# Performance work log

Measured on AMD Instinct MI355X. Metric: run time of the kernel, lower is better.

Reference implementation:

```python
import jax, jax.numpy as jnp
import numpy as np

N, F_IN, H, OUT, E = 32000, 256, 4, 64, 512000
NEG_SLOPE = 0.2


def setup_inputs() -> dict:
    key = jax.random.key(0)
    ks = jax.random.split(key, 7)
    return {
        "feat": jax.random.normal(ks[0], (N, F_IN), dtype=jnp.float32),
        "dist": jax.random.uniform(ks[1], (E, 1, 1), dtype=jnp.float32),
        "W": jax.random.normal(ks[2], (F_IN, H * OUT), dtype=jnp.float32) * (1.0 / np.sqrt(F_IN)),
        "w_att_src": jax.random.normal(ks[3], (1, H, OUT), dtype=jnp.float32) * 0.1,
        "w_att_dst": jax.random.normal(ks[4], (1, H, OUT), dtype=jnp.float32) * 0.1,
        "src": jax.random.randint(ks[5], (E,), 0, N, dtype=jnp.int32),
        "dst": jax.random.randint(ks[6], (E,), 0, N, dtype=jnp.int32),
    }


def reference(feat, dist, W, w_att_src, w_att_dst, src, dst):
    n = feat.shape[0]
    # dense projection (no bias, no activation) then split heads: [N, H, OUT]
    ft = (feat @ W).reshape(n, H, OUT)
    # per-node attention logits: [N, H, 1]
    e_src = jnp.sum(ft * w_att_src, axis=-1, keepdims=True)
    e_dst = jnp.sum(ft * w_att_dst, axis=-1, keepdims=True)
    # edge logits via u_add_v gather: [E, H, 1]
    e = e_src[src] + e_dst[dst]
    e = jnp.where(e >= 0, e, NEG_SLOPE * e)  # leaky relu
    # edge softmax normalized over incoming edges of each dst node
    emax = jax.ops.segment_max(e, dst, num_segments=n)          # [N, H, 1]
    ex = jnp.exp(e - emax[dst])
    denom = jax.ops.segment_sum(ex, dst, num_segments=n)        # [N, H, 1]
    a = (ex / denom[dst]) * dist                                # [E, H, 1]
    # message = u_mul_e, aggregate = sum over incoming edges
    m = ft[src] * a                                             # [E, H, OUT]
    out = jax.ops.segment_sum(m, dst, num_segments=n)           # [N, H, OUT]
    return out.reshape(n, H * OUT)
```

## Files before the change

### kernel.cpp

```cpp
#include <hip/hip_runtime.h>

#define F_IN 256
#define NHEAD 4
#define DOUT 64
#define FOUT 256
#define NEG_SLOPE 0.2f
#define BCAP 64
#define PREP_BLKS 16
#define QSTRIDE 272

typedef __attribute__((ext_vector_type(8))) short bf16x8;
typedef __attribute__((ext_vector_type(4))) float f32x4;

__device__ __forceinline__ unsigned short f2bf(float x) {
    unsigned u = __float_as_uint(x);
    return (unsigned short)((u + 0x7FFFu + ((u >> 16) & 1u)) >> 16);
}

__global__ __launch_bounds__(256) void k_prep_zero(
    const float* __restrict__ W, unsigned short* __restrict__ Wt,
    int* __restrict__ cnt, int n)
{
    if (blockIdx.x < PREP_BLKS) {
        __shared__ float tile[64][65];
        int bi = blockIdx.x >> 2, bj = blockIdx.x & 3;
        int t = threadIdx.x;
        int r0 = t >> 6, c = t & 63;
#pragma unroll
        for (int it = 0; it < 16; ++it) {
            int r = it * 4 + r0;
            tile[r][c] = W[(size_t)(bi * 64 + r) * FOUT + bj * 64 + c];
        }
        __syncthreads();
#pragma unroll
        for (int it = 0; it < 16; ++it) {
            int r = it * 4 + r0;
            Wt[(size_t)(bj * 64 + r) * F_IN + bi * 64 + c] = f2bf(tile[c][r]);
        }
        return;
    }
    int i = (blockIdx.x - PREP_BLKS) * 256 + threadIdx.x;
    if (i < n / 4) ((int4*)cnt)[i] = make_int4(0, 0, 0, 0);
}

__global__ __launch_bounds__(256) void k_gemm_fill(
    const float* __restrict__ feat, const unsigned short* __restrict__ Wt,
    const float* __restrict__ wsrc, const float* __restrict__ wdst,
    signed char* __restrict__ qft, int2* __restrict__ pk,
    float* __restrict__ edst,
    const int* __restrict__ src, const int* __restrict__ dst,
    const float* __restrict__ dist, int* __restrict__ cnt,
    int2* __restrict__ bkt, int E_, int GB)
{
    if (blockIdx.x >= GB) {
        int e = (blockIdx.x - GB) * 256 + threadIdx.x;
        if (e >= E_) return;
        int d = dst[e];
        int p = atomicAdd(&cnt[d], 1);
        if (p < BCAP) bkt[(size_t)d * BCAP + p] = make_int2(src[e], __float_as_int(dist[e]));
        return;
    }

    __shared__ unsigned short A_lds[64 * 40];
    __shared__ signed char q_lds[64 * QSTRIDE];
    const int m0   = blockIdx.x * 64;
    const int tid  = threadIdx.x;
    const int w    = tid >> 6;
    const int lane = tid & 63;
    const int l15  = lane & 15, l4 = lane >> 4;

    const int srow = tid >> 2, skg = tid & 3;
    const float* gA = &feat[(size_t)(m0 + srow) * F_IN + skg * 8];
    unsigned short* sA = &A_lds[srow * 40 + skg * 8];

    f32x4 acc[4][4];
#pragma unroll
    for (int mi = 0; mi < 4; ++mi)
#pragma unroll
        for (int ni = 0; ni < 4; ++ni)
            acc[mi][ni] = (f32x4){0.f, 0.f, 0.f, 0.f};

    for (int ks = 0; ks < F_IN / 32; ++ks) {
        float4 a0 = *(const float4*)(gA + ks * 32);
        float4 a1 = *(const float4*)(gA + ks * 32 + 4);
        if (ks) __syncthreads();
        bf16x8 pkv;
        pkv[0] = (short)f2bf(a0.x); pkv[1] = (short)f2bf(a0.y);
        pkv[2] = (short)f2bf(a0.z); pkv[3] = (short)f2bf(a0.w);
        pkv[4] = (short)f2bf(a1.x); pkv[5] = (short)f2bf(a1.y);
        pkv[6] = (short)f2bf(a1.z); pkv[7] = (short)f2bf(a1.w);
        *(bf16x8*)sA = pkv;
        __syncthreads();

        bf16x8 bfr[4];
#pragma unroll
        for (int ni = 0; ni < 4; ++ni)
            bfr[ni] = *(const bf16x8*)&Wt[(size_t)(w * 64 + ni * 16 + l15) * F_IN + ks * 32 + l4 * 8];
        bf16x8 afr[4];
#pragma unroll
        for (int mi = 0; mi < 4; ++mi)
            afr[mi] = *(const bf16x8*)&A_lds[(mi * 16 + l15) * 40 + l4 * 8];
#pragma unroll
        for (int mi = 0; mi < 4; ++mi)
#pragma unroll
            for (int ni = 0; ni < 4; ++ni)
                acc[mi][ni] = __builtin_amdgcn_mfma_f32_16x16x32_bf16(
                    afr[mi], bfr[ni], acc[mi][ni], 0, 0, 0);
    }

    float wsv[4], wdv[4];
#pragma unroll
    for (int ni = 0; ni < 4; ++ni) {
        wsv[ni] = wsrc[w * 64 + ni * 16 + l15];
        wdv[ni] = wdst[w * 64 + ni * 16 + l15];
    }
#pragma unroll
    for (int mi = 0; mi < 4; ++mi) {
#pragma unroll
        for (int r = 0; r < 4; ++r) {
            int row = m0 + mi * 16 + l4 * 4 + r;
            float ps = 0.f, pd = 0.f, mx = 0.f;
#pragma unroll
            for (int ni = 0; ni < 4; ++ni) {
                float v = acc[mi][ni][r];
                ps += v * wsv[ni];
                pd += v * wdv[ni];
                mx = fmaxf(mx, fabsf(v));
            }
#pragma unroll
            for (int m = 1; m < 16; m <<= 1) {
                ps += __shfl_xor(ps, m);
                pd += __shfl_xor(pd, m);
                mx = fmaxf(mx, __shfl_xor(mx, m));
            }
            float inv_s = 127.0f / fmaxf(mx, 1e-20f);
#pragma unroll
            for (int ni = 0; ni < 4; ++ni) {
                int q = __float2int_rn(acc[mi][ni][r] * inv_s);
                q = (q > 127) ? 127 : ((q < -127) ? -127 : q);
                q_lds[(mi * 16 + l4 * 4 + r) * QSTRIDE + w * 64 + ni * 16 + l15] = (signed char)q;
            }
            if (l15 == 0) {
                pk[row * NHEAD + w] = make_int2(__float_as_int(ps),
                                                __float_as_int(mx * (1.0f / 127.0f)));
                edst[row * NHEAD + w] = pd;
            }
        }
    }
    __syncthreads();
    {
        int row = tid >> 2, seg = tid & 3;
        const int4* s = (const int4*)&q_lds[row * QSTRIDE + seg * 64];
        int4* d4 = (int4*)&qft[(size_t)(m0 + row) * FOUT + seg * 64];
        d4[0] = s[0]; d4[1] = s[1]; d4[2] = s[2]; d4[3] = s[3];
    }
}

__global__ __launch_bounds__(256) void k_agg(
    const int* __restrict__ cnt, const int2* __restrict__ bkt,
    const int2* __restrict__ pk, const float* __restrict__ edst,
    const signed char* __restrict__ qft, float* __restrict__ out, int n)
{
    int node = blockIdx.x * 4 + (threadIdx.x >> 6);
    if (node >= n) return;
    int lane = threadIdx.x & 63;
    int g = lane >> 4;
    int l = lane & 15;
    int h = l >> 2;
    int cn = cnt[node]; if (cn > BCAP) cn = BCAP;
    const int2* b = &bkt[(size_t)node * BCAP];
    float ed = edst[node * NHEAD + h];

    float denom = 0.f;
    float acc[16];
#pragma unroll
    for (int k = 0; k < 16; ++k) acc[k] = 0.f;

    for (int i = 0; i < cn; i += 8) {
        int jA = i + g, jB = i + 4 + g;
        bool vA = jA < cn, vB = jB < cn;
        int2 cA = vA ? b[jA] : make_int2(0, 0);
        int2 cB = vB ? b[jB] : make_int2(0, 0);

        int4 rA = *(const int4*)&qft[(size_t)cA.x * FOUT + l * 16];
        int4 rB = *(const int4*)&qft[(size_t)cB.x * FOUT + l * 16];
        int2 pA2 = pk[cA.x * NHEAD + h];
        int2 pB2 = pk[cB.x * NHEAD + h];

        float lgA = __int_as_float(pA2.x) + ed;
        float lgB = __int_as_float(pB2.x) + ed;
        lgA = (lgA >= 0.f) ? lgA : NEG_SLOPE * lgA;
        lgB = (lgB >= 0.f) ? lgB : NEG_SLOPE * lgB;
        float pA = vA ? __expf(lgA) : 0.f;
        float pB = vB ? __expf(lgB) : 0.f;
        denom += pA + pB;

        float aA = pA * __int_as_float(cA.y) * __int_as_float(pA2.y);
        float aB = pB * __int_as_float(cB.y) * __int_as_float(pB2.y);

        const unsigned wA[4] = {(unsigned)rA.x, (unsigned)rA.y, (unsigned)rA.z, (unsigned)rA.w};
        const unsigned wB[4] = {(unsigned)rB.x, (unsigned)rB.y, (unsigned)rB.z, (unsigned)rB.w};
#pragma unroll
        for (int wd = 0; wd < 4; ++wd) {
            acc[wd * 4 + 0] += (float)(signed char)(wA[wd])       * aA + (float)(signed char)(wB[wd])       * aB;
            acc[wd * 4 + 1] += (float)(signed char)(wA[wd] >> 8)  * aA + (float)(signed char)(wB[wd] >> 8)  * aB;
            acc[wd * 4 + 2] += (float)(signed char)(wA[wd] >> 16) * aA + (float)(signed char)(wB[wd] >> 16) * aB;
            acc[wd * 4 + 3] += (float)(signed char)(wA[wd] >> 24) * aA + (float)(signed char)(wB[wd] >> 24) * aB;
        }
    }

#pragma unroll
    for (int m = 16; m < 64; m <<= 1) {
        denom += __shfl_xor(denom, m);
#pragma unroll
        for (int k = 0; k < 16; ++k) acc[k] += __shfl_xor(acc[k], m);
    }

    float inv = (denom > 0.f) ? 1.f / denom : 0.f;
    if (g == 0) {
#pragma unroll
        for (int q4 = 0; q4 < 4; ++q4) {
            float4 o = { acc[q4 * 4 + 0] * inv, acc[q4 * 4 + 1] * inv,
                         acc[q4 * 4 + 2] * inv, acc[q4 * 4 + 3] * inv };
            *(float4*)&out[(size_t)node * FOUT + l * 16 + q4 * 4] = o;
        }
    }
}

extern "C" void kernel_launch(void* const* d_in, const int* in_sizes, int n_in,
                              void* d_out, int out_size, void* d_ws, size_t ws_size,
                              hipStream_t stream)
{
    const float* feat = (const float*)d_in[0];
    const float* dist = (const float*)d_in[1];
    const float* W    = (const float*)d_in[2];
    const float* wsrc = (const float*)d_in[3];
    const float* wdst = (const float*)d_in[4];
    const int*   src  = (const int*)d_in[5];
    const int*   dst  = (const int*)d_in[6];
    float* out = (float*)d_out;

    const int n  = in_sizes[0] / F_IN;
    const int E_ = in_sizes[5];

    float* ws = (float*)d_ws;
    size_t off = 0;
    signed char* qft = (signed char*)(ws + off); off += (size_t)n * FOUT / 4;
    unsigned short* Wt = (unsigned short*)(ws + off); off += (size_t)F_IN * FOUT / 2;
    int2*  pk   = (int2*)(ws + off); off += (size_t)n * NHEAD * 2;
    float* edst = ws + off; off += (size_t)n * NHEAD;
    int2*  bkt  = (int2*)(ws + off); off += (size_t)n * BCAP * 2;
    int*   cnt  = (int*)(ws + off);  off += (size_t)n;

    const int ZB = (n / 4 + 255) / 256;
    k_prep_zero<<<PREP_BLKS + ZB, 256, 0, stream>>>(W, Wt, cnt, n);

    const int GB = n / 64;
    const int FB = (E_ + 255) / 256;
    k_gemm_fill<<<GB + FB, 256, 0, stream>>>(feat, Wt, wsrc, wdst, qft, pk, edst,
                                             src, dst, dist, cnt, bkt, E_, GB);

    k_agg<<<(n + 3) / 4, 256, 0, stream>>>(cnt, bkt, pk, edst, qft, out, n);
}
```

Before: 70.49 us.

## Split int8 quantization out of GEMM into a separate quant kernel via bf16 buffer

The GEMM kernel now writes projected features as bf16 straight to global memory and per-node source logits to a separate array. It no longer does the per-row max reduction, the int8 quantization through LDS or the staged copy-out. A new kernel reads the bf16 rows, computes a per-head max from the bf16 bit patterns, quantizes to int8 and packs the scale with the source logit. This shortens the GEMM epilogue and frees its LDS, at the cost of an extra launch, an extra bf16 round trip through global memory, scattered 2-byte stores, and quantization from bf16-rounded values.

```diff
diff --git a/kernel.cpp b/kernel.cpp
--- a/kernel.cpp
+++ b/kernel.cpp
@@ -7,7 +7,6 @@
 #define NEG_SLOPE 0.2f
 #define BCAP 64
 #define PREP_BLKS 16
-#define QSTRIDE 272
 
 typedef __attribute__((ext_vector_type(8))) short bf16x8;
 typedef __attribute__((ext_vector_type(4))) float f32x4;
@@ -46,7 +45,7 @@
 __global__ __launch_bounds__(256) void k_gemm_fill(
     const float* __restrict__ feat, const unsigned short* __restrict__ Wt,
     const float* __restrict__ wsrc, const float* __restrict__ wdst,
-    signed char* __restrict__ qft, int2* __restrict__ pk,
+    unsigned short* __restrict__ ftb, float* __restrict__ esrc,
     float* __restrict__ edst,
     const int* __restrict__ src, const int* __restrict__ dst,
     const float* __restrict__ dist, int* __restrict__ cnt,
@@ -62,7 +61,6 @@
     }
 
     __shared__ unsigned short A_lds[64 * 40];
-    __shared__ signed char q_lds[64 * QSTRIDE];
     const int m0   = blockIdx.x * 64;
     const int tid  = threadIdx.x;
     const int w    = tid >> 6;
@@ -119,41 +117,67 @@
 #pragma unroll
         for (int r = 0; r < 4; ++r) {
             int row = m0 + mi * 16 + l4 * 4 + r;
-            float ps = 0.f, pd = 0.f, mx = 0.f;
+            float ps = 0.f, pd = 0.f;
 #pragma unroll
             for (int ni = 0; ni < 4; ++ni) {
                 float v = acc[mi][ni][r];
+                ftb[(size_t)row * FOUT + w * 64 + ni * 16 + l15] = f2bf(v);
                 ps += v * wsv[ni];
                 pd += v * wdv[ni];
-                mx = fmaxf(mx, fabsf(v));
             }
 #pragma unroll
             for (int m = 1; m < 16; m <<= 1) {
                 ps += __shfl_xor(ps, m);
                 pd += __shfl_xor(pd, m);
-                mx = fmaxf(mx, __shfl_xor(mx, m));
-            }
-            float inv_s = 127.0f / fmaxf(mx, 1e-20f);
-#pragma unroll
-            for (int ni = 0; ni < 4; ++ni) {
-                int q = __float2int_rn(acc[mi][ni][r] * inv_s);
-                q = (q > 127) ? 127 : ((q < -127) ? -127 : q);
-                q_lds[(mi * 16 + l4 * 4 + r) * QSTRIDE + w * 64 + ni * 16 + l15] = (signed char)q;
             }
             if (l15 == 0) {
-                pk[row * NHEAD + w] = make_int2(__float_as_int(ps),
-                                                __float_as_int(mx * (1.0f / 127.0f)));
+                esrc[row * NHEAD + w] = ps;
                 edst[row * NHEAD + w] = pd;
             }
         }
     }
-    __syncthreads();
-    {
-        int row = tid >> 2, seg = tid & 3;
-        const int4* s = (const int4*)&q_lds[row * QSTRIDE + seg * 64];
-        int4* d4 = (int4*)&qft[(size_t)(m0 + row) * FOUT + seg * 64];
-        d4[0] = s[0]; d4[1] = s[1]; d4[2] = s[2]; d4[3] = s[3];
-    }
+}
+
+__global__ __launch_bounds__(256) void k_quant(
+    const unsigned short* __restrict__ ftb, const float* __restrict__ esrc,
+    signed char* __restrict__ qft, int2* __restrict__ pk, int n)
+{
+    int t = blockIdx.x * 256 + threadIdx.x;
+    if (t >= n * NHEAD) return;
+    const uint4* s = (const uint4*)(ftb + (size_t)t * DOUT);
+    uint4 d[8];
+#pragma unroll
+    for (int i = 0; i < 8; ++i) d[i] = s[i];
+
+    unsigned mb = 0;
+#pragma unroll
+    for (int i = 0; i < 8; ++i) {
+        unsigned w0 = d[i].x, w1 = d[i].y, w2 = d[i].z, w3 = d[i].w;
+        mb = max(mb, max(w0 & 0x7FFFu, (w0 >> 16) & 0x7FFFu));
+        mb = max(mb, max(w1 & 0x7FFFu, (w1 >> 16) & 0x7FFFu));
+        mb = max(mb, max(w2 & 0x7FFFu, (w2 >> 16) & 0x7FFFu));
+        mb = max(mb, max(w3 & 0x7FFFu, (w3 >> 16) & 0x7FFFu));
+    }
+    float mx = __uint_as_float(mb << 16);
+    float inv_s = 127.0f / fmaxf(mx, 1e-20f);
+
+    unsigned qw[16];
+    const unsigned* wsrc32 = (const unsigned*)d;
+#pragma unroll
+    for (int j = 0; j < 16; ++j) {
+        unsigned a = wsrc32[j * 2], b = wsrc32[j * 2 + 1];
+        int q0 = __float2int_rn(__uint_as_float(a << 16) * inv_s);
+        int q1 = __float2int_rn(__uint_as_float(a & 0xFFFF0000u) * inv_s);
+        int q2 = __float2int_rn(__uint_as_float(b << 16) * inv_s);
+        int q3 = __float2int_rn(__uint_as_float(b & 0xFFFF0000u) * inv_s);
+        qw[j] = (q0 & 255) | ((q1 & 255) << 8) | ((q2 & 255) << 16) | ((q3 & 255) << 24);
+    }
+    int4* o = (int4*)(qft + (size_t)t * DOUT);
+#pragma unroll
+    for (int j = 0; j < 4; ++j)
+        o[j] = make_int4(qw[j * 4], qw[j * 4 + 1], qw[j * 4 + 2], qw[j * 4 + 3]);
+
+    pk[t] = make_int2(__float_as_int(esrc[t]), __float_as_int(mx * (1.0f / 127.0f)));
 }
 
 __global__ __launch_bounds__(256) void k_agg(
@@ -245,10 +269,12 @@
 
     float* ws = (float*)d_ws;
     size_t off = 0;
+    unsigned short* ftb = (unsigned short*)(ws + off); off += (size_t)n * FOUT / 2;
     signed char* qft = (signed char*)(ws + off); off += (size_t)n * FOUT / 4;
     unsigned short* Wt = (unsigned short*)(ws + off); off += (size_t)F_IN * FOUT / 2;
+    float* esrc = ws + off; off += (size_t)n * NHEAD;
+    float* edst = ws + off; off += (size_t)n * NHEAD;
     int2*  pk   = (int2*)(ws + off); off += (size_t)n * NHEAD * 2;
-    float* edst = ws + off; off += (size_t)n * NHEAD;
     int2*  bkt  = (int2*)(ws + off); off += (size_t)n * BCAP * 2;
     int*   cnt  = (int*)(ws + off);  off += (size_t)n;
 
@@ -257,8 +283,10 @@
 
     const int GB = n / 64;
     const int FB = (E_ + 255) / 256;
-    k_gemm_fill<<<GB + FB, 256, 0, stream>>>(feat, Wt, wsrc, wdst, qft, pk, edst,
+    k_gemm_fill<<<GB + FB, 256, 0, stream>>>(feat, Wt, wsrc, wdst, ftb, esrc, edst,
                                              src, dst, dist, cnt, bkt, E_, GB);
 
+    k_quant<<<(n * NHEAD + 255) / 256, 256, 0, stream>>>(ftb, esrc, qft, pk, n);
+
     k_agg<<<(n + 3) / 4, 256, 0, stream>>>(cnt, bkt, pk, edst, qft, out, n);
 }
```

Measured after the change: 76.75 us. 8.9% more time.
